# Optimization experiments

Measured on AMD Instinct MI355X. Metric: run time of the kernel, lower is better.

Reference implementation:

```python
import jax, jax.numpy as jnp
import numpy as np

NUM_EMB = 1024
EMB_DIM = 256
BETA = 0.25


def setup_inputs() -> dict:
    key = jax.random.key(0)
    k1, k2 = jax.random.split(key)
    z = jax.random.normal(k1, (64, 32, 32, EMB_DIM), dtype=jnp.float32)
    # RandomUniform(-1/N, 1/N) init, shape (embedding_dimension, number_embeddings)
    embeddings = jax.random.uniform(
        k2, (EMB_DIM, NUM_EMB), dtype=jnp.float32,
        minval=-1.0 / NUM_EMB, maxval=1.0 / NUM_EMB)
    return {"z": z, "embeddings": embeddings}


def reference(z, embeddings):
    beta = BETA
    z_flat = z.reshape(-1, EMB_DIM)                      # [N, D]
    # squared L2 distances via ||z||^2 + ||e||^2 - 2 z @ e
    distances = (jnp.sum(z_flat ** 2, axis=1, keepdims=True)
                 + jnp.sum(embeddings ** 2, axis=0)
                 - 2.0 * (z_flat @ embeddings))          # [N, K]
    encoding_indices = jnp.argmin(distances, axis=1)     # [N] int
    quantized = embeddings.T[encoding_indices].reshape(z.shape)  # gather rows of e^T
    vq_loss = jnp.mean((quantized - jax.lax.stop_gradient(z)) ** 2)
    commitment_loss = beta * jnp.mean((jax.lax.stop_gradient(quantized) - z) ** 2)
    quantized_st = z + jax.lax.stop_gradient(quantized - z)  # straight-through
    # perplexity from codebook usage histogram
    counts = jnp.zeros((NUM_EMB,), dtype=distances.dtype).at[encoding_indices].add(1.0)
    avg_probs = counts / encoding_indices.shape[0]
    perplexity = jnp.exp(-jnp.sum(avg_probs * jnp.log(avg_probs + 1e-10)))
    return (quantized_st, encoding_indices, vq_loss, commitment_loss, perplexity)
```

## Files before the change

### kernel.cpp

```cpp
#include <hip/hip_runtime.h>
#include <math.h>

#define NUM_EMB 1024
#define EMB_DIM 256
#define NROWS   65536
#define NTHREADS 256
#define EPSF 1.5e-3f
#define GCAP 524288

#define OFF_IDX  16777216
#define OFF_VQ   16842752

#define WS_C2    0
#define WS_HIST  4096
#define WS_LOSS  8192
#define WS_GCNT  8196
#define WS_R2    8448
#define WS_SLOT  270592
#define WS_ETF   794880
#define WS_ETB   1843456
#define WS_GLIST 2367744

typedef __attribute__((ext_vector_type(8))) short bf16x8;
typedef __attribute__((ext_vector_type(4))) float f32x4;

__device__ __forceinline__ unsigned short f2bf(float x) {
  unsigned u = __float_as_uint(x);
  unsigned r = (u + 0x7FFFu + ((u >> 16) & 1u)) >> 16;
  return (unsigned short)r;
}

__global__ __launch_bounds__(NTHREADS) void vq_prep(
    const float* __restrict__ emb, float* __restrict__ cvec,
    int* __restrict__ hist, float* __restrict__ loss, int* __restrict__ gcnt) {
  int k = blockIdx.x * blockDim.x + threadIdx.x;
  if (k < NUM_EMB) {
    float s = 0.f;
    for (int d = 0; d < EMB_DIM; ++d) {
      float v = emb[d * NUM_EMB + k];
      s = __fadd_rn(s, __fmul_rn(v, v));
    }
    cvec[k] = s;
    hist[k] = 0;
  }
  if (k == 0) { *loss = 0.f; *gcnt = 0; }
}

__global__ __launch_bounds__(NTHREADS) void vq_tr(
    const float* __restrict__ emb, float* __restrict__ embTf,
    unsigned short* __restrict__ embTbf) {
  __shared__ float t[64][65];
  const int kt = blockIdx.x & 15, dt = blockIdx.x >> 4;
  const int tid = threadIdx.x;
  #pragma unroll
  for (int it = 0; it < 16; ++it) {
    int i = tid + it * NTHREADS, r = i >> 6, c = i & 63;
    t[r][c] = emb[(dt * 64 + r) * NUM_EMB + kt * 64 + c];
  }
  __syncthreads();
  #pragma unroll
  for (int it = 0; it < 16; ++it) {
    int i = tid + it * NTHREADS, r = i >> 6, c = i & 63;
    float v = t[c][r];
    embTf[(kt * 64 + r) * EMB_DIM + dt * 64 + c] = v;
    embTbf[(kt * 64 + r) * EMB_DIM + dt * 64 + c] = f2bf(v);
  }
}

__global__ __launch_bounds__(NTHREADS) void vq_r2k(
    const float* __restrict__ z, float* __restrict__ r2out) {
  __shared__ float zc[64][36];
  __shared__ float pmm[64][2][4];
  const int tid = threadIdx.x;
  const int n0 = blockIdx.x * 64;
  const float* zrow = z + (size_t)n0 * EMB_DIM;
  const int prow = tid >> 2, pm = tid & 3;
  float racc[2][2] = {{0.f, 0.f}, {0.f, 0.f}};
  for (int dc = 0; dc < 8; ++dc) {
    __syncthreads();
    #pragma unroll
    for (int it = 0; it < 2; ++it) {
      int i = tid + it * NTHREADS, row = i >> 3, f4 = i & 7;
      *(float4*)(&zc[row][f4 * 4]) = *(const float4*)(zrow + row * EMB_DIM + dc * 32 + f4 * 4);
    }
    __syncthreads();
    const int half = dc >> 2;
    #pragma unroll
    for (int q = 0; q < 4; ++q)
      #pragma unroll
      for (int jj = 0; jj < 2; ++jj) {
        float v = zc[prow][(pm * 2 + jj) + 8 * q];
        racc[half][jj] = __fadd_rn(racc[half][jj], __fmul_rn(v, v));
      }
  }
  pmm[prow][0][pm] = __fadd_rn(racc[0][0], racc[0][1]);
  pmm[prow][1][pm] = __fadd_rn(racc[1][0], racc[1][1]);
  __syncthreads();
  if (tid < 64) {
    float h0 = __fadd_rn(__fadd_rn(pmm[tid][0][0], pmm[tid][0][1]),
                         __fadd_rn(pmm[tid][0][2], pmm[tid][0][3]));
    float h1 = __fadd_rn(__fadd_rn(pmm[tid][1][0], pmm[tid][1][1]),
                         __fadd_rn(pmm[tid][1][2], pmm[tid][1][3]));
    r2out[n0 + tid] = __fadd_rn(h0, h1);
  }
}

__global__ __launch_bounds__(NTHREADS, 2) void vq_mfma(
    const float* __restrict__ z, const unsigned short* __restrict__ embTbf,
    const float* __restrict__ cvec, unsigned long long* __restrict__ slots,
    int* __restrict__ gcnt, unsigned int* __restrict__ glist) {
  __shared__ unsigned short zc[64][264];
  __shared__ unsigned short Bl[256][56];
  __shared__ float c2s[NUM_EMB];
  __shared__ int rowminb[64];
  __shared__ int lcnt, lbase, lcount;
  __shared__ unsigned int llist[512];

  const int tid = threadIdx.x;
  const int wave = tid >> 6, lane = tid & 63;
  const int quad = lane >> 4, l15 = lane & 15;
  const int n0 = blockIdx.x * 64;

  for (int i = tid; i < NUM_EMB; i += NTHREADS) c2s[i] = cvec[i] + 1.0f;
  if (tid < 64) {
    rowminb[tid] = 0x7F000000;
    slots[n0 + tid] = ~0ULL;
  }
  #pragma unroll
  for (int it = 0; it < 16; ++it) {
    int g = tid + it * NTHREADS, row = g >> 6, f4 = g & 63;
    float4 v = *(const float4*)(z + (size_t)(n0 + row) * EMB_DIM + f4 * 4);
    ushort4 b;
    b.x = f2bf(v.x); b.y = f2bf(v.y); b.z = f2bf(v.z); b.w = f2bf(v.w);
    *(ushort4*)(&zc[row][f4 * 4]) = b;
  }

  for (int j = 0; j < 4; ++j) {
    f32x4 acc[4][4];
    #pragma unroll
    for (int rt = 0; rt < 4; ++rt)
      #pragma unroll
      for (int ct = 0; ct < 4; ++ct)
        acc[rt][ct] = (f32x4){0.f, 0.f, 0.f, 0.f};

    for (int kc = 0; kc < 8; ++kc) {
      __syncthreads();
      #pragma unroll
      for (int it = 0; it < 4; ++it) {
        int nn = (tid >> 2) + it * 64, seg = tid & 3;
        uint4 v = *(const uint4*)(embTbf + (size_t)(j * 256 + nn) * EMB_DIM + kc * 32 + seg * 8);
        *(uint4*)(&Bl[nn][seg * 8]) = v;
      }
      __syncthreads();
      bf16x8 av[4], bv[4];
      #pragma unroll
      for (int rt = 0; rt < 4; ++rt)
        av[rt] = *(const bf16x8*)(&zc[rt * 16 + l15][kc * 32 + quad * 8]);
      #pragma unroll
      for (int ct = 0; ct < 4; ++ct)
        bv[ct] = *(const bf16x8*)(&Bl[wave * 64 + ct * 16 + l15][quad * 8]);
      #pragma unroll
      for (int rt = 0; rt < 4; ++rt)
        #pragma unroll
        for (int ct = 0; ct < 4; ++ct)
          acc[rt][ct] = __builtin_amdgcn_mfma_f32_16x16x32_bf16(av[rt], bv[ct], acc[rt][ct], 0, 0, 0);
    }

    #pragma unroll
    for (int rt = 0; rt < 4; ++rt)
      #pragma unroll
      for (int reg = 0; reg < 4; ++reg) {
        float m = 1e30f;
        #pragma unroll
        for (int ct = 0; ct < 4; ++ct) {
          int k = j * 256 + wave * 64 + ct * 16 + l15;
          float d = fmaf(-2.f, acc[rt][ct][reg], c2s[k]);
          m = fminf(m, d);
        }
        #pragma unroll
        for (int off = 1; off < 16; off <<= 1)
          m = fminf(m, __shfl_xor(m, off));
        if (l15 == 0)
          atomicMin(&rowminb[rt * 16 + quad * 4 + reg], __float_as_int(m));
      }
    if (tid == 0) lcnt = 0;
    __syncthreads();

    #pragma unroll
    for (int rt = 0; rt < 4; ++rt)
      #pragma unroll
      for (int reg = 0; reg < 4; ++reg) {
        int rowl = rt * 16 + quad * 4 + reg;
        float fmin = __int_as_float(rowminb[rowl]);
        #pragma unroll
        for (int ct = 0; ct < 4; ++ct) {
          int k = j * 256 + wave * 64 + ct * 16 + l15;
          float d = fmaf(-2.f, acc[rt][ct][reg], c2s[k]);
          if (d <= fmin + EPSF) {
            int id = atomicAdd(&lcnt, 1);
            if (id < 512) llist[id] = ((unsigned)(n0 + rowl) << 10) | (unsigned)k;
          }
        }
      }
    __syncthreads();
    if (tid == 0) {
      int c = lcnt < 512 ? lcnt : 512;
      lcount = c;
      lbase = atomicAdd(gcnt, c);
    }
    __syncthreads();
    for (int i = tid; i < lcount; i += NTHREADS)
      if (lbase + i < GCAP) glist[lbase + i] = llist[i];
    __syncthreads();
  }
}

__global__ __launch_bounds__(NTHREADS) void vq_refine(
    const float* __restrict__ z, const float* __restrict__ embTf,
    const float* __restrict__ r2, const float* __restrict__ cvec,
    const int* __restrict__ gcnt, const unsigned int* __restrict__ glist,
    unsigned long long* __restrict__ slots) {
  int n = *gcnt; if (n > GCAP) n = GCAP;
  for (int i = blockIdx.x * NTHREADS + threadIdx.x; i < n;
       i += gridDim.x * NTHREADS) {
    unsigned e = glist[i];
    int grow = (int)(e >> 10), k = (int)(e & 1023);
    const float* zr = z + (size_t)grow * EMB_DIM;
    const float* er = embTf + (size_t)k * EMB_DIM;
    float s = 0.f;
    for (int d = 0; d < EMB_DIM; ++d)
      s = fmaf(zr[d], er[d], s);
    float dist = __fsub_rn(__fadd_rn(r2[grow], cvec[k]), __fmul_rn(2.0f, s));
    unsigned long long key =
        ((unsigned long long)__float_as_uint(dist) << 32) | (unsigned)k;
    atomicMin(&slots[grow], key);
  }
}

__global__ __launch_bounds__(NTHREADS) void vq_epi(
    const float* __restrict__ z, const float* __restrict__ embTf,
    const unsigned long long* __restrict__ slots,
    float* __restrict__ out, int* __restrict__ hist, float* __restrict__ loss) {
  __shared__ int ks[64];
  __shared__ float wsum[4];
  const int tid = threadIdx.x;
  const int n0 = blockIdx.x * 64;
  const float* zrow = z + (size_t)n0 * EMB_DIM;
  if (tid < 64) {
    int k = (int)(slots[n0 + tid] & 1023ULL);
    ks[tid] = k;
    out[OFF_IDX + n0 + tid] = (float)k;
    atomicAdd(&hist[k], 1);
  }
  __syncthreads();
  float sumsq = 0.f;
  #pragma unroll
  for (int it = 0; it < 16; ++it) {
    int g = tid + it * NTHREADS;
    int row = g >> 6;
    int d = (g & 63) * 4;
    int k = ks[row];
    float4 zv = *(const float4*)(zrow + row * EMB_DIM + d);
    float4 q = *(const float4*)(embTf + (size_t)k * EMB_DIM + d);
    float4 df;
    df.x = q.x - zv.x; df.y = q.y - zv.y; df.z = q.z - zv.z; df.w = q.w - zv.w;
    sumsq = fmaf(df.x, df.x, sumsq);
    sumsq = fmaf(df.y, df.y, sumsq);
    sumsq = fmaf(df.z, df.z, sumsq);
    sumsq = fmaf(df.w, df.w, sumsq);
    *(float4*)(out + (size_t)(n0 + row) * EMB_DIM + d) = q;
  }
  #pragma unroll
  for (int off = 32; off > 0; off >>= 1) sumsq += __shfl_down(sumsq, off);
  if ((tid & 63) == 0) wsum[tid >> 6] = sumsq;
  __syncthreads();
  if (tid == 0) atomicAdd(loss, wsum[0] + wsum[1] + wsum[2] + wsum[3]);
}

__global__ __launch_bounds__(NTHREADS) void vq_finalize(
    const int* __restrict__ hist, const float* __restrict__ loss,
    float* __restrict__ out) {
  __shared__ float ws[4];
  int tid = threadIdx.x;
  float s = 0.f;
  for (int k = tid; k < NUM_EMB; k += NTHREADS) {
    float p = (float)hist[k] * (1.0f / 65536.0f);
    s += p * logf(p + 1e-10f);
  }
  #pragma unroll
  for (int off = 32; off > 0; off >>= 1) s += __shfl_down(s, off);
  if ((tid & 63) == 0) ws[tid >> 6] = s;
  __syncthreads();
  if (tid == 0) {
    float tot = ws[0] + ws[1] + ws[2] + ws[3];
    float vq = *loss * (1.0f / 16777216.0f);
    out[OFF_VQ + 0] = vq;
    out[OFF_VQ + 1] = 0.25f * vq;
    out[OFF_VQ + 2] = expf(-tot);
  }
}

extern "C" void kernel_launch(void* const* d_in, const int* in_sizes, int n_in,
                              void* d_out, int out_size, void* d_ws, size_t ws_size,
                              hipStream_t stream) {
  const float* z   = (const float*)d_in[0];
  const float* emb = (const float*)d_in[1];
  float* out = (float*)d_out;
  char* ws = (char*)d_ws;
  float* cvec   = (float*)(ws + WS_C2);
  int*   hist   = (int*)(ws + WS_HIST);
  float* loss   = (float*)(ws + WS_LOSS);
  int*   gcnt   = (int*)(ws + WS_GCNT);
  float* r2     = (float*)(ws + WS_R2);
  unsigned long long* slots = (unsigned long long*)(ws + WS_SLOT);
  float* embTf  = (float*)(ws + WS_ETF);
  unsigned short* embTbf = (unsigned short*)(ws + WS_ETB);
  unsigned int* glist = (unsigned int*)(ws + WS_GLIST);

  vq_prep<<<4, NTHREADS, 0, stream>>>(emb, cvec, hist, loss, gcnt);
  vq_tr<<<64, NTHREADS, 0, stream>>>(emb, embTf, embTbf);
  vq_r2k<<<NROWS / 64, NTHREADS, 0, stream>>>(z, r2);
  vq_mfma<<<NROWS / 64, NTHREADS, 0, stream>>>(z, embTbf, cvec, slots, gcnt, glist);
  vq_refine<<<512, NTHREADS, 0, stream>>>(z, embTf, r2, cvec, gcnt, glist, slots);
  vq_epi<<<NROWS / 64, NTHREADS, 0, stream>>>(z, embTf, slots, out, hist, loss);
  vq_finalize<<<1, NTHREADS, 0, stream>>>(hist, loss, out);
}
```

Before: 317.5 us.

## Enlarge MFMA block to 256 rows with 16 waves, swizzled LDS, prefetched B

The bf16 distance kernel now runs 1024-thread blocks covering 256 rows, with waves split into 4 row groups × 4 column groups. Each codebook tile loaded into LDS is therefore reused by four times as many rows. The z tile is stored with an XOR swizzle to avoid LDS bank conflicts. The next B chunk is register-prefetched from global memory while the current one computes, and the codebook norms are held in registers instead of LDS. Costs include higher LDS use (about 128KB for zc), fewer blocks in flight, and 1024-thread barriers.

```diff
diff --git a/kernel.cpp b/kernel.cpp
--- a/kernel.cpp
+++ b/kernel.cpp
@@ -5,6 +5,7 @@
 #define EMB_DIM 256
 #define NROWS   65536
 #define NTHREADS 256
+#define MTHREADS 1024
 #define EPSF 1.5e-3f
 #define GCAP 524288
 
@@ -105,35 +106,44 @@
   }
 }
 
-__global__ __launch_bounds__(NTHREADS, 2) void vq_mfma(
+__global__ __launch_bounds__(MTHREADS) void vq_mfma(
     const float* __restrict__ z, const unsigned short* __restrict__ embTbf,
     const float* __restrict__ cvec, unsigned long long* __restrict__ slots,
     int* __restrict__ gcnt, unsigned int* __restrict__ glist) {
-  __shared__ unsigned short zc[64][264];
-  __shared__ unsigned short Bl[256][56];
-  __shared__ float c2s[NUM_EMB];
-  __shared__ int rowminb[64];
+  __shared__ unsigned short zc[256][256];
+  __shared__ unsigned short Bl[256][40];
+  __shared__ int rowminb[256];
+  __shared__ unsigned int llist[2048];
   __shared__ int lcnt, lbase, lcount;
-  __shared__ unsigned int llist[512];
 
   const int tid = threadIdx.x;
-  const int wave = tid >> 6, lane = tid & 63;
+  const int lane = tid & 63, wave = tid >> 6;
   const int quad = lane >> 4, l15 = lane & 15;
-  const int n0 = blockIdx.x * 64;
-
-  for (int i = tid; i < NUM_EMB; i += NTHREADS) c2s[i] = cvec[i] + 1.0f;
-  if (tid < 64) {
+  const int rg = wave >> 2, cg = wave & 3;
+  const int n0 = blockIdx.x * 256;
+
+  if (tid < 256) {
     rowminb[tid] = 0x7F000000;
     slots[n0 + tid] = ~0ULL;
   }
-  #pragma unroll
-  for (int it = 0; it < 16; ++it) {
-    int g = tid + it * NTHREADS, row = g >> 6, f4 = g & 63;
-    float4 v = *(const float4*)(z + (size_t)(n0 + row) * EMB_DIM + f4 * 4);
-    ushort4 b;
-    b.x = f2bf(v.x); b.y = f2bf(v.y); b.z = f2bf(v.z); b.w = f2bf(v.w);
-    *(ushort4*)(&zc[row][f4 * 4]) = b;
-  }
+
+  #pragma unroll
+  for (int it = 0; it < 8; ++it) {
+    int g = tid + it * MTHREADS, row = g >> 5, u = g & 31;
+    const float* src = z + (size_t)(n0 + row) * EMB_DIM + u * 8;
+    float4 a = *(const float4*)src;
+    float4 b = *(const float4*)(src + 4);
+    uint4 w;
+    w.x = ((unsigned)f2bf(a.y) << 16) | f2bf(a.x);
+    w.y = ((unsigned)f2bf(a.w) << 16) | f2bf(a.z);
+    w.z = ((unsigned)f2bf(b.y) << 16) | f2bf(b.x);
+    w.w = ((unsigned)f2bf(b.w) << 16) | f2bf(b.z);
+    *(uint4*)(&zc[row][(u ^ (row & 7)) * 8]) = w;
+  }
+
+  const int bn = tid >> 2, bseg = tid & 3;
+  const size_t bofs = (size_t)bn * EMB_DIM + (size_t)bseg * 8;
+  uint4 bpre = *(const uint4*)(embTbf + bofs);
 
   for (int j = 0; j < 4; ++j) {
     f32x4 acc[4][4];
@@ -142,23 +152,28 @@
       #pragma unroll
       for (int ct = 0; ct < 4; ++ct)
         acc[rt][ct] = (f32x4){0.f, 0.f, 0.f, 0.f};
+    float c2r[4];
+    #pragma unroll
+    for (int ct = 0; ct < 4; ++ct)
+      c2r[ct] = cvec[j * 256 + cg * 64 + ct * 16 + l15] + 1.0f;
 
     for (int kc = 0; kc < 8; ++kc) {
       __syncthreads();
-      #pragma unroll
-      for (int it = 0; it < 4; ++it) {
-        int nn = (tid >> 2) + it * 64, seg = tid & 3;
-        uint4 v = *(const uint4*)(embTbf + (size_t)(j * 256 + nn) * EMB_DIM + kc * 32 + seg * 8);
-        *(uint4*)(&Bl[nn][seg * 8]) = v;
+      *(uint4*)(&Bl[bn][bseg * 8]) = bpre;
+      __syncthreads();
+      int c = j * 8 + kc + 1;
+      if (c < 32)
+        bpre = *(const uint4*)(embTbf + (size_t)(c >> 3) * 65536 +
+                               (size_t)(c & 7) * 32 + bofs);
+      bf16x8 av[4], bv[4];
+      #pragma unroll
+      for (int rt = 0; rt < 4; ++rt) {
+        int row = rg * 64 + rt * 16 + l15;
+        av[rt] = *(const bf16x8*)(&zc[row][((kc * 4 + quad) ^ (l15 & 7)) * 8]);
       }
-      __syncthreads();
-      bf16x8 av[4], bv[4];
-      #pragma unroll
-      for (int rt = 0; rt < 4; ++rt)
-        av[rt] = *(const bf16x8*)(&zc[rt * 16 + l15][kc * 32 + quad * 8]);
       #pragma unroll
       for (int ct = 0; ct < 4; ++ct)
-        bv[ct] = *(const bf16x8*)(&Bl[wave * 64 + ct * 16 + l15][quad * 8]);
+        bv[ct] = *(const bf16x8*)(&Bl[cg * 64 + ct * 16 + l15][quad * 8]);
       #pragma unroll
       for (int rt = 0; rt < 4; ++rt)
         #pragma unroll
@@ -173,15 +188,14 @@
         float m = 1e30f;
         #pragma unroll
         for (int ct = 0; ct < 4; ++ct) {
-          int k = j * 256 + wave * 64 + ct * 16 + l15;
-          float d = fmaf(-2.f, acc[rt][ct][reg], c2s[k]);
+          float d = fmaf(-2.f, acc[rt][ct][reg], c2r[ct]);
           m = fminf(m, d);
         }
         #pragma unroll
         for (int off = 1; off < 16; off <<= 1)
           m = fminf(m, __shfl_xor(m, off));
         if (l15 == 0)
-          atomicMin(&rowminb[rt * 16 + quad * 4 + reg], __float_as_int(m));
+          atomicMin(&rowminb[rg * 64 + rt * 16 + quad * 4 + reg], __float_as_int(m));
       }
     if (tid == 0) lcnt = 0;
     __syncthreads();
@@ -190,26 +204,26 @@
     for (int rt = 0; rt < 4; ++rt)
       #pragma unroll
       for (int reg = 0; reg < 4; ++reg) {
-        int rowl = rt * 16 + quad * 4 + reg;
+        int rowl = rg * 64 + rt * 16 + quad * 4 + reg;
         float fmin = __int_as_float(rowminb[rowl]);
         #pragma unroll
         for (int ct = 0; ct < 4; ++ct) {
-          int k = j * 256 + wave * 64 + ct * 16 + l15;
-          float d = fmaf(-2.f, acc[rt][ct][reg], c2s[k]);
+          int k = j * 256 + cg * 64 + ct * 16 + l15;
+          float d = fmaf(-2.f, acc[rt][ct][reg], c2r[ct]);
           if (d <= fmin + EPSF) {
             int id = atomicAdd(&lcnt, 1);
-            if (id < 512) llist[id] = ((unsigned)(n0 + rowl) << 10) | (unsigned)k;
+            if (id < 2048) llist[id] = ((unsigned)(n0 + rowl) << 10) | (unsigned)k;
           }
         }
       }
     __syncthreads();
     if (tid == 0) {
-      int c = lcnt < 512 ? lcnt : 512;
+      int c = lcnt < 2048 ? lcnt : 2048;
       lcount = c;
       lbase = atomicAdd(gcnt, c);
     }
     __syncthreads();
-    for (int i = tid; i < lcount; i += NTHREADS)
+    for (int i = tid; i < lcount; i += MTHREADS)
       if (lbase + i < GCAP) glist[lbase + i] = llist[i];
     __syncthreads();
   }
@@ -320,7 +334,7 @@
   vq_prep<<<4, NTHREADS, 0, stream>>>(emb, cvec, hist, loss, gcnt);
   vq_tr<<<64, NTHREADS, 0, stream>>>(emb, embTf, embTbf);
   vq_r2k<<<NROWS / 64, NTHREADS, 0, stream>>>(z, r2);
-  vq_mfma<<<NROWS / 64, NTHREADS, 0, stream>>>(z, embTbf, cvec, slots, gcnt, glist);
+  vq_mfma<<<NROWS / 256, MTHREADS, 0, stream>>>(z, embTbf, cvec, slots, gcnt, glist);
   vq_refine<<<512, NTHREADS, 0, stream>>>(z, embTf, r2, cvec, gcnt, glist, slots);
   vq_epi<<<NROWS / 64, NTHREADS, 0, stream>>>(z, embTf, slots, out, hist, loss);
   vq_finalize<<<1, NTHREADS, 0, stream>>>(hist, loss, out);
```

Result: faster. 291.1 us (-8.3%).
